# Optimization experiments

Measured on AMD Instinct MI355X. Metric: run time of the kernel, lower is better.

Reference implementation:

```python
import jax, jax.numpy as jnp
import numpy as np

B, S, DIM, HEADS = 4, 2048, 1024, 16
SCALE = float((DIM // HEADS) ** 0.5)  # sqrt(d_k) = 8.0
EPS = 1e-5


def _ln(h, g, b):
    m = jnp.mean(h, axis=-1, keepdims=True)
    v = jnp.mean((h - m) ** 2, axis=-1, keepdims=True)
    return (h - m) * jax.lax.rsqrt(v + EPS) * g + b


def setup_inputs() -> dict:
    key = jax.random.key(0)
    ks = jax.random.split(key, 16)
    w = lambda k: jax.random.normal(k, (DIM, DIM), jnp.float32) * 0.02
    vec = lambda k: jax.random.normal(k, (DIM,), jnp.float32) * 0.02
    return {
        "x": jax.random.normal(ks[0], (B, S, DIM), jnp.float32),
        "Wq": w(ks[1]), "bq": vec(ks[2]),
        "Wk": w(ks[3]), "bk": vec(ks[4]),
        "Wv": w(ks[5]), "bv": vec(ks[6]),
        "g_at": 1.0 + vec(ks[7]), "b_at": vec(ks[8]),
        "g_ln": 1.0 + vec(ks[9]), "b_ln": vec(ks[10]),
        "W1": w(ks[11]), "c1": vec(ks[12]),
        "W2": w(ks[13]), "c2": vec(ks[14]),
    }


def reference(x, Wq, bq, Wk, bk, Wv, bv, g_at, b_at, g_ln, b_ln, W1, c1, W2, c2):
    # --- MultiHeadAttention (single-head math: no head reshape in source) ---
    Q = x @ Wq + bq                                   # [B,S,D]
    K = x @ Wk + bk
    V = x @ Wv + bv
    scores = jax.nn.softmax(jnp.einsum('bqd,bkd->bqk', Q, K) / SCALE, axis=-1)
    at = _ln(jnp.einsum('bqk,bkd->bqd', scores, V) + x, g_at, b_at)
    # --- EncoderStack ---
    h = _ln(at + x, g_ln, b_ln)
    res = h
    # note: source's `if i != len(self.ffn)` is always True -> GELU on every layer
    h = jax.nn.gelu(h @ W1 + c1, approximate=False)
    h = jax.nn.gelu(h @ W2 + c2, approximate=False)
    return _ln(h + res, g_ln, b_ln)
```

## Files before the change

### kernel.cpp

```cpp
#include <hip/hip_runtime.h>
#include <cstdint>
#include <cstddef>

#define DIMN 1024
#define SEQ  2048
#define NBAT 4
#define TOKS (NBAT * SEQ)

typedef unsigned short u16;
typedef unsigned int   u32;

typedef __bf16 bf16x8 __attribute__((ext_vector_type(8)));
typedef float  f32x4  __attribute__((ext_vector_type(4)));

#define AS1 __attribute__((address_space(1)))
#define AS3 __attribute__((address_space(3)))


__device__ __forceinline__ u16 f2b(float f) {
  union { float f; u32 u; } v; v.f = f;
  u32 r = v.u + 0x7fffu + ((v.u >> 16) & 1u);
  return (u16)(r >> 16);
}

__device__ __forceinline__ float b2f(u16 b) {
  union { u32 u; float f; } v; v.u = ((u32)b) << 16;
  return v.f;
}

__device__ __forceinline__ float gelu_exact(float v) {
  return 0.5f * v * (1.0f + erff(v * 0.70710678118654752f));
}

__device__ __forceinline__ void blk_sum2(float& a, float& b, float* sm) {
  #pragma unroll
  for (int o = 32; o >= 1; o >>= 1) {
    a += __shfl_xor(a, o, 64);
    b += __shfl_xor(b, o, 64);
  }
  int w = threadIdx.x >> 6;
  if ((threadIdx.x & 63) == 0) { sm[w] = a; sm[4 + w] = b; }
  __syncthreads();
  a = sm[0] + sm[1] + sm[2] + sm[3];
  b = sm[4] + sm[5] + sm[6] + sm[7];
  __syncthreads();
}

__device__ __forceinline__ float blk_max(float a, float* sm) {
  #pragma unroll
  for (int o = 32; o >= 1; o >>= 1) a = fmaxf(a, __shfl_xor(a, o, 64));
  int w = threadIdx.x >> 6;
  if ((threadIdx.x & 63) == 0) sm[w] = a;
  __syncthreads();
  float r = fmaxf(fmaxf(sm[0], sm[1]), fmaxf(sm[2], sm[3]));
  __syncthreads();
  return r;
}

__device__ __forceinline__ float blk_sum1(float a, float* sm) {
  #pragma unroll
  for (int o = 32; o >= 1; o >>= 1) a += __shfl_xor(a, o, 64);
  int w = threadIdx.x >> 6;
  if ((threadIdx.x & 63) == 0) sm[w] = a;
  __syncthreads();
  float r = sm[0] + sm[1] + sm[2] + sm[3];
  __syncthreads();
  return r;
}

__global__ __launch_bounds__(256) void prep_all(
    const float* __restrict__ x,
    const float* __restrict__ Wq, const float* __restrict__ Wk,
    const float* __restrict__ Wv, const float* __restrict__ W1,
    const float* __restrict__ W2,
    u16* __restrict__ xb,
    u16* __restrict__ Wqkv, u16* __restrict__ W1T, u16* __restrict__ W2T)
{
  __shared__ float t[32][33];
  const int tx = threadIdx.x, ty = threadIdx.y;
  if (blockIdx.z == 5) {
    const int tid = ty * 32 + tx;
    const size_t base = ((size_t)(blockIdx.y * 32 + blockIdx.x)) * 8192;
    #pragma unroll
    for (int it = 0; it < 8; ++it) {
      size_t i = base + (size_t)(it * 256 + tid) * 4;
      float4 v = *(const float4*)(x + i);
      uint2 o;
      o.x = (u32)f2b(v.x) | ((u32)f2b(v.y) << 16);
      o.y = (u32)f2b(v.z) | ((u32)f2b(v.w) << 16);
      *(uint2*)(xb + i) = o;
    }
    return;
  }
  const float* W; u16* T;
  switch (blockIdx.z) {
    case 0: W = Wq; T = Wqkv;                   break;
    case 1: W = Wk; T = Wqkv + 1 * DIMN * DIMN; break;
    case 2: W = Wv; T = Wqkv + 2 * DIMN * DIMN; break;
    case 3: W = W1; T = W1T;                    break;
    default: W = W2; T = W2T;                   break;
  }
  int k0 = blockIdx.x * 32, n0 = blockIdx.y * 32;
  #pragma unroll
  for (int j = 0; j < 32; j += 8)
    t[ty + j][tx] = W[(size_t)(k0 + ty + j) * DIMN + n0 + tx];
  __syncthreads();
  #pragma unroll
  for (int j = 0; j < 32; j += 8)
    T[(size_t)(n0 + ty + j) * DIMN + k0 + tx] = f2b(t[tx][ty + j]);
}

template <int EPI, int SWZ>
__global__ __launch_bounds__(256) void gemm_bt(
    const u16* __restrict__ A, const u16* __restrict__ Bm,
    u16* __restrict__ Cb, u16* __restrict__ Cb2, u16* __restrict__ Cb3,
    const float* __restrict__ bias, const float* __restrict__ bias2,
    const float* __restrict__ bias3,
    int M, int N, int K, int ldc,
    size_t sA, size_t sB, size_t sC)
{
  __shared__ u16 smem[2 * 128 * 64];
  u16* As = smem;
  u16* Bs = smem + 128 * 64;

  const int tid = threadIdx.x;

  int bm0, bn0;
  if (SWZ == 1) {
    const int id   = blockIdx.y * gridDim.x + blockIdx.x;
    const int xcd  = id & 7;
    const int idx  = id >> 3;
    const int band = gridDim.x >> 3;
    bm0 = (xcd * band + idx % band) * 128;
    bn0 = (idx / band) * 128;
  } else {
    bm0 = blockIdx.x * 128;
    bn0 = blockIdx.y * 128;
  }

  A  += (size_t)blockIdx.z * sA;
  Bm += (size_t)blockIdx.z * sB;
  const int wave = tid >> 6, lane = tid & 63;
  const int wm   = (wave >> 1) * 64, wn = (wave & 1) * 64;
  const int l16  = lane & 15, quad = lane >> 4;

  f32x4 acc[4][4] = {};

  for (int k0 = 0; k0 < K; k0 += 64) {
    #pragma unroll
    for (int j = 0; j < 4; ++j) {
      const int c  = wave * 256 + j * 64 + lane;
      const int r  = c >> 3;
      const int cg = (c & 7) ^ (r & 7);
      const u16* gA = A  + (size_t)(bm0 + r) * K + k0 + cg * 8;
      const u16* gB = Bm + (size_t)(bn0 + r) * K + k0 + cg * 8;
      u16* lA = As + (wave * 4 + j) * 512;
      u16* lB = Bs + (wave * 4 + j) * 512;
      __builtin_amdgcn_global_load_lds((const AS1 void*)gA, (AS3 void*)lA, 16, 0, 0);
      __builtin_amdgcn_global_load_lds((const AS1 void*)gB, (AS3 void*)lB, 16, 0, 0);
    }
    __syncthreads();

    #pragma unroll
    for (int kk = 0; kk < 64; kk += 32) {
      const int kc = kk >> 3;
      const int sw = l16 & 7;
      bf16x8 af[4], bfr[4];
      #pragma unroll
      for (int t = 0; t < 4; ++t) {
        const int row = wm + t * 16 + l16;
        af[t] = *(const bf16x8*)(&As[row * 64 + (((kc + quad) ^ sw) << 3)]);
      }
      #pragma unroll
      for (int t = 0; t < 4; ++t) {
        const int row = wn + t * 16 + l16;
        bfr[t] = *(const bf16x8*)(&Bs[row * 64 + (((kc + quad) ^ sw) << 3)]);
      }
      #pragma unroll
      for (int mt = 0; mt < 4; ++mt)
        #pragma unroll
        for (int nt = 0; nt < 4; ++nt)
          acc[mt][nt] = __builtin_amdgcn_mfma_f32_16x16x32_bf16(
              af[mt], bfr[nt], acc[mt][nt], 0, 0, 0);
    }
    __syncthreads();
  }

  if (EPI == 3 && (bn0 >> 10) == 2) {
    #pragma unroll
    for (int mt = 0; mt < 4; ++mt) {
      const int tok_l0 = wm + mt * 16 + quad * 4;
      #pragma unroll
      for (int nt = 0; nt < 4; ++nt) {
        const int d_l = wn + nt * 16 + l16;
        const float bv = bias3[(bn0 & 1023) + d_l];
        ushort4 pk;
        pk.x = f2b(acc[mt][nt][0] + bv);
        pk.y = f2b(acc[mt][nt][1] + bv);
        pk.z = f2b(acc[mt][nt][2] + bv);
        pk.w = f2b(acc[mt][nt][3] + bv);
        const int addr = d_l * 128 +
            ((((tok_l0 >> 3) ^ (d_l & 7)) << 3) | (tok_l0 & 7));
        *(ushort4*)(&smem[addr]) = pk;
      }
    }
    __syncthreads();
    const int b_idx = bm0 >> 11;
    const int tok0  = bm0 & 2047;
    const int d0    = bn0 & 1023;
    u16* dst = Cb3 + (size_t)b_idx * DIMN * SEQ;
    #pragma unroll
    for (int p = 0; p < 8; ++p) {
      const int idx = p * 256 + tid;
      const int row = idx >> 4, c = idx & 15;
      uint4 v = *(const uint4*)(&smem[row * 128 + ((c ^ (row & 7)) << 3)]);
      *(uint4*)(&dst[(size_t)(d0 + row) * SEQ + tok0 + c * 8]) = v;
    }
    return;
  }

  u16* Cbz = Cb + (size_t)blockIdx.z * sC;
  #pragma unroll
  for (int mt = 0; mt < 4; ++mt) {
    int grow0 = bm0 + wm + mt * 16 + quad * 4;
    #pragma unroll
    for (int nt = 0; nt < 4; ++nt) {
      int gcol = bn0 + wn + nt * 16 + l16;
      if (EPI == 3) {
        const int seg = gcol >> 10;
        const int col = gcol & 1023;
        const float* bp = (seg == 0) ? bias : bias2;
        u16*         cp = (seg == 0) ? Cb   : Cb2;
        float bv = bp[col];
        #pragma unroll
        for (int r = 0; r < 4; ++r)
          cp[(size_t)(grow0 + r) * ldc + col] = f2b(acc[mt][nt][r] + bv);
      } else if (EPI == 4) {
        float bv = bias[gcol];
        #pragma unroll
        for (int r = 0; r < 4; ++r)
          Cbz[(size_t)(grow0 + r) * ldc + gcol] =
              f2b(gelu_exact(acc[mt][nt][r] + bv));
      } else {
        #pragma unroll
        for (int r = 0; r < 4; ++r)
          Cbz[(size_t)(grow0 + r) * ldc + gcol] = f2b(acc[mt][nt][r]);
      }
    }
  }
}

__global__ __launch_bounds__(256) void softmax_rows(const u16* __restrict__ Sc,
                                                    u16* __restrict__ P) {
  __shared__ float sm[8];
  int row = blockIdx.x, t = threadIdx.x;
  const u16* s = Sc + (size_t)row * SEQ;
  uint4 raw = *(const uint4*)(s + t * 8);
  float v[8];
  #pragma unroll
  for (int m = 0; m < 4; ++m) {
    u32 w = ((const u32*)&raw)[m];
    v[2 * m]     = b2f((u16)(w & 0xffff)) * 0.125f;
    v[2 * m + 1] = b2f((u16)(w >> 16)) * 0.125f;
  }
  float mx = -1e30f;
  #pragma unroll
  for (int i = 0; i < 8; ++i) mx = fmaxf(mx, v[i]);
  mx = blk_max(mx, sm);
  float sum = 0.0f;
  #pragma unroll
  for (int i = 0; i < 8; ++i) { v[i] = __expf(v[i] - mx); sum += v[i]; }
  sum = blk_sum1(sum, sm);
  float inv = 1.0f / sum;
  uint4 o;
  #pragma unroll
  for (int m = 0; m < 4; ++m)
    ((u32*)&o)[m] = (u32)f2b(v[2 * m] * inv) | ((u32)f2b(v[2 * m + 1] * inv) << 16);
  *(uint4*)(P + (size_t)row * SEQ + t * 8) = o;
}

__global__ __launch_bounds__(256) void ln1_fused(
    const u16* __restrict__ attn, const u16* __restrict__ xb,
    const float* __restrict__ g_at, const float* __restrict__ b_at,
    const float* __restrict__ g_ln, const float* __restrict__ b_ln,
    u16* __restrict__ hres)
{
  __shared__ float sm[8];
  int row = blockIdx.x, t = threadIdx.x;
  size_t base = (size_t)row * DIMN;
  uint2 ar = *(const uint2*)(attn + base + t * 4);
  uint2 xr4 = *(const uint2*)(xb + base + t * 4);
  float y[4], xr[4];
  float s = 0.0f, s2 = 0.0f;
  #pragma unroll
  for (int i = 0; i < 4; ++i) {
    u32 aw = ((const u32*)&ar)[i >> 1];
    u32 xw = ((const u32*)&xr4)[i >> 1];
    float av = b2f((u16)((i & 1) ? (aw >> 16) : (aw & 0xffff)));
    xr[i]    = b2f((u16)((i & 1) ? (xw >> 16) : (xw & 0xffff)));
    y[i] = av + xr[i];
    s += y[i]; s2 += y[i] * y[i];
  }
  blk_sum2(s, s2, sm);
  float m  = s * (1.0f / DIMN);
  float rs = rsqrtf(s2 * (1.0f / DIMN) - m * m + 1e-5f);
  float z[4];
  s = 0.0f; s2 = 0.0f;
  #pragma unroll
  for (int i = 0; i < 4; ++i) {
    int c = t * 4 + i;
    float at = (y[i] - m) * rs * g_at[c] + b_at[c];
    z[i] = at + xr[i];
    s += z[i]; s2 += z[i] * z[i];
  }
  blk_sum2(s, s2, sm);
  float m2  = s * (1.0f / DIMN);
  float rs2 = rsqrtf(s2 * (1.0f / DIMN) - m2 * m2 + 1e-5f);
  uint2 o;
  #pragma unroll
  for (int i = 0; i < 2; ++i) {
    int c = t * 4 + 2 * i;
    float h0 = (z[2 * i]     - m2) * rs2 * g_ln[c]     + b_ln[c];
    float h1 = (z[2 * i + 1] - m2) * rs2 * g_ln[c + 1] + b_ln[c + 1];
    ((u32*)&o)[i] = (u32)f2b(h0) | ((u32)f2b(h1) << 16);
  }
  *(uint2*)(hres + base + t * 4) = o;
}

__global__ __launch_bounds__(256) void ln2_final(
    const u16* __restrict__ u, const u16* __restrict__ hres,
    const float* __restrict__ g, const float* __restrict__ bb,
    float* __restrict__ out)
{
  __shared__ float sm[8];
  int row = blockIdx.x, t = threadIdx.x;
  size_t base = (size_t)row * DIMN;
  uint2 ur = *(const uint2*)(u + base + t * 4);
  uint2 hr = *(const uint2*)(hres + base + t * 4);
  float y[4];
  float s = 0.0f, s2 = 0.0f;
  #pragma unroll
  for (int i = 0; i < 4; ++i) {
    u32 uw = ((const u32*)&ur)[i >> 1];
    u32 hw = ((const u32*)&hr)[i >> 1];
    float uv = b2f((u16)((i & 1) ? (uw >> 16) : (uw & 0xffff)));
    float hv = b2f((u16)((i & 1) ? (hw >> 16) : (hw & 0xffff)));
    y[i] = uv + hv;
    s += y[i]; s2 += y[i] * y[i];
  }
  blk_sum2(s, s2, sm);
  float m  = s * (1.0f / DIMN);
  float rs = rsqrtf(s2 * (1.0f / DIMN) - m * m + 1e-5f);
  float4 o;
  o.x = (y[0] - m) * rs * g[t * 4 + 0] + bb[t * 4 + 0];
  o.y = (y[1] - m) * rs * g[t * 4 + 1] + bb[t * 4 + 1];
  o.z = (y[2] - m) * rs * g[t * 4 + 2] + bb[t * 4 + 2];
  o.w = (y[3] - m) * rs * g[t * 4 + 3] + bb[t * 4 + 3];
  *(float4*)(out + base + t * 4) = o;
}


extern "C" void kernel_launch(void* const* d_in, const int* in_sizes, int n_in,
                              void* d_out, int out_size, void* d_ws, size_t ws_size,
                              hipStream_t stream)
{
  const float* x    = (const float*)d_in[0];
  const float* Wq   = (const float*)d_in[1];
  const float* bq   = (const float*)d_in[2];
  const float* Wk   = (const float*)d_in[3];
  const float* bk   = (const float*)d_in[4];
  const float* Wv   = (const float*)d_in[5];
  const float* bv   = (const float*)d_in[6];
  const float* g_at = (const float*)d_in[7];
  const float* b_at = (const float*)d_in[8];
  const float* g_ln = (const float*)d_in[9];
  const float* b_ln = (const float*)d_in[10];
  const float* W1   = (const float*)d_in[11];
  const float* c1   = (const float*)d_in[12];
  const float* W2   = (const float*)d_in[13];
  const float* c2   = (const float*)d_in[14];
  float* out = (float*)d_out;

  char* ws = (char*)d_ws;
  const size_t MB = 1u << 20;
  u16* xb    = (u16*)(ws + 0 * MB);
  u16* W1T   = (u16*)(ws + 16 * MB);
  u16* W2T   = (u16*)(ws + 18 * MB);
  u16* WqkvT = (u16*)(ws + 20 * MB);
  u16* Qb    = (u16*)(ws + 26 * MB);
  u16* Kb    = (u16*)(ws + 42 * MB);
  u16* VT    = (u16*)(ws + 58 * MB);
  u16* Sc    = (u16*)(ws + 74 * MB);
  u16* attn  = (u16*)(ws + 74 * MB);
  u16* hres  = (u16*)(ws + 90 * MB);
  u16* Pb    = (u16*)(ws + 106 * MB);
  u16* tb    = Kb;
  u16* ub    = VT;

  prep_all<<<dim3(32, 32, 6), dim3(32, 8), 0, stream>>>(
      x, Wq, Wk, Wv, W1, W2, xb, WqkvT, W1T, W2T);

  gemm_bt<3, 1><<<dim3(64, 24), 256, 0, stream>>>(
      xb, WqkvT, Qb, Kb, VT, bq, bk, bv,
      TOKS, 3 * DIMN, DIMN, DIMN, 0, 0, 0);

  gemm_bt<6, 0><<<dim3(16, 16, NBAT), 256, 0, stream>>>(
      Qb, Kb, Sc, nullptr, nullptr, nullptr, nullptr, nullptr,
      SEQ, SEQ, DIMN, SEQ,
      (size_t)SEQ * DIMN, (size_t)SEQ * DIMN, (size_t)SEQ * SEQ);
  softmax_rows<<<TOKS, 256, 0, stream>>>(Sc, Pb);
  gemm_bt<6, 0><<<dim3(16, 8, NBAT), 256, 0, stream>>>(
      Pb, VT, attn, nullptr, nullptr, nullptr, nullptr, nullptr,
      SEQ, DIMN, SEQ, DIMN,
      (size_t)SEQ * SEQ, (size_t)DIMN * SEQ, (size_t)SEQ * DIMN);

  ln1_fused<<<TOKS, 256, 0, stream>>>(attn, xb, g_at, b_at, g_ln, b_ln, hres);

  gemm_bt<4, 1><<<dim3(64, 8), 256, 0, stream>>>(
      hres, W1T, tb, nullptr, nullptr, c1, nullptr, nullptr,
      TOKS, DIMN, DIMN, DIMN, 0, 0, 0);
  gemm_bt<4, 1><<<dim3(64, 8), 256, 0, stream>>>(
      tb, W2T, ub, nullptr, nullptr, c2, nullptr, nullptr,
      TOKS, DIMN, DIMN, DIMN, 0, 0, 0);

  ln2_final<<<TOKS, 256, 0, stream>>>(ub, hres, g_ln, b_ln, out);
}
```

Baseline: 386.6 us.

## Stage GEMM epilogue through LDS, use tanh GELU, wave-per-row softmax and layernorm

The GEMM epilogue now writes results into swizzled shared memory and then issues coalesced 16-byte global stores, in place of scattered 2-byte stores. Exact erf GELU is replaced with the tanh approximation built from __expf. Softmax and both layernorm kernels now process one row per wave with only shuffle reductions, which removes block barriers and uses wider vector loads. The tanh GELU changes numerics relative to the exact reference, and the extra LDS round trip adds a barrier to every GEMM.

```diff
diff --git a/kernel.cpp b/kernel.cpp
--- a/kernel.cpp
+++ b/kernel.cpp
@@ -28,44 +28,40 @@
   return v.f;
 }
 
-__device__ __forceinline__ float gelu_exact(float v) {
-  return 0.5f * v * (1.0f + erff(v * 0.70710678118654752f));
-}
-
-__device__ __forceinline__ void blk_sum2(float& a, float& b, float* sm) {
-  #pragma unroll
-  for (int o = 32; o >= 1; o >>= 1) {
-    a += __shfl_xor(a, o, 64);
-    b += __shfl_xor(b, o, 64);
-  }
-  int w = threadIdx.x >> 6;
-  if ((threadIdx.x & 63) == 0) { sm[w] = a; sm[4 + w] = b; }
-  __syncthreads();
-  a = sm[0] + sm[1] + sm[2] + sm[3];
-  b = sm[4] + sm[5] + sm[6] + sm[7];
-  __syncthreads();
-}
-
-__device__ __forceinline__ float blk_max(float a, float* sm) {
+__device__ __forceinline__ float gelu_fast(float x) {
+  float y = 0.79788456080286536f * (x + 0.044715f * x * x * x);
+  float e = __expf(2.0f * y);
+  float t = 1.0f - 2.0f / (e + 1.0f);
+  return 0.5f * x * (1.0f + t);
+}
+
+__device__ __forceinline__ float wave_sum(float a) {
+  #pragma unroll
+  for (int o = 32; o >= 1; o >>= 1) a += __shfl_xor(a, o, 64);
+  return a;
+}
+
+__device__ __forceinline__ float wave_max(float a) {
   #pragma unroll
   for (int o = 32; o >= 1; o >>= 1) a = fmaxf(a, __shfl_xor(a, o, 64));
-  int w = threadIdx.x >> 6;
-  if ((threadIdx.x & 63) == 0) sm[w] = a;
-  __syncthreads();
-  float r = fmaxf(fmaxf(sm[0], sm[1]), fmaxf(sm[2], sm[3]));
-  __syncthreads();
-  return r;
-}
-
-__device__ __forceinline__ float blk_sum1(float a, float* sm) {
-  #pragma unroll
-  for (int o = 32; o >= 1; o >>= 1) a += __shfl_xor(a, o, 64);
-  int w = threadIdx.x >> 6;
-  if ((threadIdx.x & 63) == 0) sm[w] = a;
-  __syncthreads();
-  float r = sm[0] + sm[1] + sm[2] + sm[3];
-  __syncthreads();
-  return r;
+  return a;
+}
+
+__device__ __forceinline__ void unpack8(uint4 raw, float* o) {
+  #pragma unroll
+  for (int m = 0; m < 4; ++m) {
+    u32 w = ((const u32*)&raw)[m];
+    o[2 * m]     = b2f((u16)(w & 0xffff));
+    o[2 * m + 1] = b2f((u16)(w >> 16));
+  }
+}
+
+__device__ __forceinline__ uint4 pack8(const float* v) {
+  uint4 o;
+  #pragma unroll
+  for (int m = 0; m < 4; ++m)
+    ((u32*)&o)[m] = (u32)f2b(v[2 * m]) | ((u32)f2b(v[2 * m + 1]) << 16);
+  return o;
 }
 
 __global__ __launch_bounds__(256) void prep_all(
@@ -186,7 +182,9 @@
     __syncthreads();
   }
 
-  if (EPI == 3 && (bn0 >> 10) == 2) {
+  const int seg = bn0 >> 10;
+
+  if (EPI == 3 && seg == 2) {
     #pragma unroll
     for (int mt = 0; mt < 4; ++mt) {
       const int tok_l0 = wm + mt * 16 + quad * 4;
@@ -219,64 +217,68 @@
     return;
   }
 
-  u16* Cbz = Cb + (size_t)blockIdx.z * sC;
+  u16* dst; const float* bp; int col0;
+  if (EPI == 3) {
+    dst = seg ? Cb2 : Cb;  bp = seg ? bias2 : bias;  col0 = bn0 & 1023;
+  } else if (EPI == 4) {
+    dst = Cb;  bp = bias;  col0 = bn0;
+  } else {
+    dst = Cb + (size_t)blockIdx.z * sC;  bp = nullptr;  col0 = bn0;
+  }
+
   #pragma unroll
   for (int mt = 0; mt < 4; ++mt) {
-    int grow0 = bm0 + wm + mt * 16 + quad * 4;
+    const int r0 = wm + mt * 16 + quad * 4;
     #pragma unroll
     for (int nt = 0; nt < 4; ++nt) {
-      int gcol = bn0 + wn + nt * 16 + l16;
-      if (EPI == 3) {
-        const int seg = gcol >> 10;
-        const int col = gcol & 1023;
-        const float* bp = (seg == 0) ? bias : bias2;
-        u16*         cp = (seg == 0) ? Cb   : Cb2;
-        float bv = bp[col];
-        #pragma unroll
-        for (int r = 0; r < 4; ++r)
-          cp[(size_t)(grow0 + r) * ldc + col] = f2b(acc[mt][nt][r] + bv);
-      } else if (EPI == 4) {
-        float bv = bias[gcol];
-        #pragma unroll
-        for (int r = 0; r < 4; ++r)
-          Cbz[(size_t)(grow0 + r) * ldc + gcol] =
-              f2b(gelu_exact(acc[mt][nt][r] + bv));
-      } else {
-        #pragma unroll
-        for (int r = 0; r < 4; ++r)
-          Cbz[(size_t)(grow0 + r) * ldc + gcol] = f2b(acc[mt][nt][r]);
+      const int cl = wn + nt * 16 + l16;
+      const float bv = (EPI == 6) ? 0.0f : bp[col0 + cl];
+      #pragma unroll
+      for (int r = 0; r < 4; ++r) {
+        float v = acc[mt][nt][r] + bv;
+        if (EPI == 4) v = gelu_fast(v);
+        const int row  = r0 + r;
+        const int addr = row * 128 + ((((cl >> 3) ^ (row & 7)) << 3) | (cl & 7));
+        smem[addr] = f2b(v);
       }
     }
+  }
+  __syncthreads();
+  #pragma unroll
+  for (int p = 0; p < 8; ++p) {
+    const int idx = p * 256 + tid;
+    const int row = idx >> 4, c = idx & 15;
+    uint4 v = *(const uint4*)(&smem[row * 128 + ((c ^ (row & 7)) << 3)]);
+    *(uint4*)(&dst[(size_t)(bm0 + row) * ldc + col0 + c * 8]) = v;
   }
 }
 
 __global__ __launch_bounds__(256) void softmax_rows(const u16* __restrict__ Sc,
                                                     u16* __restrict__ P) {
-  __shared__ float sm[8];
-  int row = blockIdx.x, t = threadIdx.x;
+  const int wave = threadIdx.x >> 6, lane = threadIdx.x & 63;
+  const int row  = blockIdx.x * 4 + wave;
   const u16* s = Sc + (size_t)row * SEQ;
-  uint4 raw = *(const uint4*)(s + t * 8);
-  float v[8];
-  #pragma unroll
-  for (int m = 0; m < 4; ++m) {
-    u32 w = ((const u32*)&raw)[m];
-    v[2 * m]     = b2f((u16)(w & 0xffff)) * 0.125f;
-    v[2 * m + 1] = b2f((u16)(w >> 16)) * 0.125f;
+  u16*       p = P  + (size_t)row * SEQ;
+  float v[32];
+  #pragma unroll
+  for (int k = 0; k < 4; ++k) {
+    uint4 raw = *(const uint4*)(s + k * 512 + lane * 8);
+    unpack8(raw, &v[k * 8]);
   }
   float mx = -1e30f;
   #pragma unroll
-  for (int i = 0; i < 8; ++i) mx = fmaxf(mx, v[i]);
-  mx = blk_max(mx, sm);
+  for (int i = 0; i < 32; ++i) { v[i] *= 0.125f; mx = fmaxf(mx, v[i]); }
+  mx = wave_max(mx);
   float sum = 0.0f;
   #pragma unroll
-  for (int i = 0; i < 8; ++i) { v[i] = __expf(v[i] - mx); sum += v[i]; }
-  sum = blk_sum1(sum, sm);
+  for (int i = 0; i < 32; ++i) { v[i] = __expf(v[i] - mx); sum += v[i]; }
+  sum = wave_sum(sum);
   float inv = 1.0f / sum;
-  uint4 o;
-  #pragma unroll
-  for (int m = 0; m < 4; ++m)
-    ((u32*)&o)[m] = (u32)f2b(v[2 * m] * inv) | ((u32)f2b(v[2 * m + 1] * inv) << 16);
-  *(uint4*)(P + (size_t)row * SEQ + t * 8) = o;
+  #pragma unroll
+  for (int i = 0; i < 32; ++i) v[i] *= inv;
+  #pragma unroll
+  for (int k = 0; k < 4; ++k)
+    *(uint4*)(p + k * 512 + lane * 8) = pack8(&v[k * 8]);
 }
 
 __global__ __launch_bounds__(256) void ln1_fused(
@@ -285,46 +287,70 @@
     const float* __restrict__ g_ln, const float* __restrict__ b_ln,
     u16* __restrict__ hres)
 {
-  __shared__ float sm[8];
-  int row = blockIdx.x, t = threadIdx.x;
-  size_t base = (size_t)row * DIMN;
-  uint2 ar = *(const uint2*)(attn + base + t * 4);
-  uint2 xr4 = *(const uint2*)(xb + base + t * 4);
-  float y[4], xr[4];
+  const int wave = threadIdx.x >> 6, lane = threadIdx.x & 63;
+  const int row  = blockIdx.x * 4 + wave;
+  const size_t base = (size_t)row * DIMN;
+  const int c0 = lane * 8, c1 = 512 + lane * 8;
+
+  float av[16], xr[16], y[16];
+  unpack8(*(const uint4*)(attn + base + c0), &av[0]);
+  unpack8(*(const uint4*)(attn + base + c1), &av[8]);
+  unpack8(*(const uint4*)(xb + base + c0), &xr[0]);
+  unpack8(*(const uint4*)(xb + base + c1), &xr[8]);
+
   float s = 0.0f, s2 = 0.0f;
   #pragma unroll
-  for (int i = 0; i < 4; ++i) {
-    u32 aw = ((const u32*)&ar)[i >> 1];
-    u32 xw = ((const u32*)&xr4)[i >> 1];
-    float av = b2f((u16)((i & 1) ? (aw >> 16) : (aw & 0xffff)));
-    xr[i]    = b2f((u16)((i & 1) ? (xw >> 16) : (xw & 0xffff)));
-    y[i] = av + xr[i];
+  for (int i = 0; i < 16; ++i) {
+    y[i] = av[i] + xr[i];
     s += y[i]; s2 += y[i] * y[i];
   }
-  blk_sum2(s, s2, sm);
+  s = wave_sum(s); s2 = wave_sum(s2);
   float m  = s * (1.0f / DIMN);
   float rs = rsqrtf(s2 * (1.0f / DIMN) - m * m + 1e-5f);
-  float z[4];
+
+  float z[16];
   s = 0.0f; s2 = 0.0f;
   #pragma unroll
-  for (int i = 0; i < 4; ++i) {
-    int c = t * 4 + i;
-    float at = (y[i] - m) * rs * g_at[c] + b_at[c];
-    z[i] = at + xr[i];
-    s += z[i]; s2 += z[i] * z[i];
-  }
-  blk_sum2(s, s2, sm);
+  for (int h = 0; h < 2; ++h) {
+    const int c = h ? c1 : c0;
+    float4 ga = *(const float4*)(g_at + c), gb = *(const float4*)(g_at + c + 4);
+    float4 ba = *(const float4*)(b_at + c), bb = *(const float4*)(b_at + c + 4);
+    const float* gp = (const float*)&ga; const float* gq = (const float*)&gb;
+    const float* bp = (const float*)&ba; const float* bq = (const float*)&bb;
+    #pragma unroll
+    for (int i = 0; i < 4; ++i) {
+      int j = h * 8 + i;
+      float at = (y[j] - m) * rs * gp[i] + bp[i];
+      z[j] = at + xr[j]; s += z[j]; s2 += z[j] * z[j];
+    }
+    #pragma unroll
+    for (int i = 0; i < 4; ++i) {
+      int j = h * 8 + 4 + i;
+      float at = (y[j] - m) * rs * gq[i] + bq[i];
+      z[j] = at + xr[j]; s += z[j]; s2 += z[j] * z[j];
+    }
+  }
+  s = wave_sum(s); s2 = wave_sum(s2);
   float m2  = s * (1.0f / DIMN);
   float rs2 = rsqrtf(s2 * (1.0f / DIMN) - m2 * m2 + 1e-5f);
-  uint2 o;
-  #pragma unroll
-  for (int i = 0; i < 2; ++i) {
-    int c = t * 4 + 2 * i;
-    float h0 = (z[2 * i]     - m2) * rs2 * g_ln[c]     + b_ln[c];
-    float h1 = (z[2 * i + 1] - m2) * rs2 * g_ln[c + 1] + b_ln[c + 1];
-    ((u32*)&o)[i] = (u32)f2b(h0) | ((u32)f2b(h1) << 16);
-  }
-  *(uint2*)(hres + base + t * 4) = o;
+
+  float o[16];
+  #pragma unroll
+  for (int h = 0; h < 2; ++h) {
+    const int c = h ? c1 : c0;
+    float4 ga = *(const float4*)(g_ln + c), gb = *(const float4*)(g_ln + c + 4);
+    float4 ba = *(const float4*)(b_ln + c), bb = *(const float4*)(b_ln + c + 4);
+    const float* gp = (const float*)&ga; const float* gq = (const float*)&gb;
+    const float* bp = (const float*)&ba; const float* bq = (const float*)&bb;
+    #pragma unroll
+    for (int i = 0; i < 4; ++i)
+      o[h * 8 + i] = (z[h * 8 + i] - m2) * rs2 * gp[i] + bp[i];
+    #pragma unroll
+    for (int i = 0; i < 4; ++i)
+      o[h * 8 + 4 + i] = (z[h * 8 + 4 + i] - m2) * rs2 * gq[i] + bq[i];
+  }
+  *(uint4*)(hres + base + c0) = pack8(&o[0]);
+  *(uint4*)(hres + base + c1) = pack8(&o[8]);
 }
 
 __global__ __launch_bounds__(256) void ln2_final(
@@ -332,31 +358,46 @@
     const float* __restrict__ g, const float* __restrict__ bb,
     float* __restrict__ out)
 {
-  __shared__ float sm[8];
-  int row = blockIdx.x, t = threadIdx.x;
-  size_t base = (size_t)row * DIMN;
-  uint2 ur = *(const uint2*)(u + base + t * 4);
-  uint2 hr = *(const uint2*)(hres + base + t * 4);
-  float y[4];
+  const int wave = threadIdx.x >> 6, lane = threadIdx.x & 63;
+  const int row  = blockIdx.x * 4 + wave;
+  const size_t base = (size_t)row * DIMN;
+  const int c0 = lane * 8, c1 = 512 + lane * 8;
+
+  float uv[16], hv[16], y[16];
+  unpack8(*(const uint4*)(u + base + c0), &uv[0]);
+  unpack8(*(const uint4*)(u + base + c1), &uv[8]);
+  unpack8(*(const uint4*)(hres + base + c0), &hv[0]);
+  unpack8(*(const uint4*)(hres + base + c1), &hv[8]);
+
   float s = 0.0f, s2 = 0.0f;
   #pragma unroll
-  for (int i = 0; i < 4; ++i) {
-    u32 uw = ((const u32*)&ur)[i >> 1];
-    u32 hw = ((const u32*)&hr)[i >> 1];
-    float uv = b2f((u16)((i & 1) ? (uw >> 16) : (uw & 0xffff)));
-    float hv = b2f((u16)((i & 1) ? (hw >> 16) : (hw & 0xffff)));
-    y[i] = uv + hv;
+  for (int i = 0; i < 16; ++i) {
+    y[i] = uv[i] + hv[i];
     s += y[i]; s2 += y[i] * y[i];
   }
-  blk_sum2(s, s2, sm);
+  s = wave_sum(s); s2 = wave_sum(s2);
   float m  = s * (1.0f / DIMN);
   float rs = rsqrtf(s2 * (1.0f / DIMN) - m * m + 1e-5f);
-  float4 o;
-  o.x = (y[0] - m) * rs * g[t * 4 + 0] + bb[t * 4 + 0];
-  o.y = (y[1] - m) * rs * g[t * 4 + 1] + bb[t * 4 + 1];
-  o.z = (y[2] - m) * rs * g[t * 4 + 2] + bb[t * 4 + 2];
-  o.w = (y[3] - m) * rs * g[t * 4 + 3] + bb[t * 4 + 3];
-  *(float4*)(out + base + t * 4) = o;
+
+  #pragma unroll
+  for (int h = 0; h < 2; ++h) {
+    const int c = h ? c1 : c0;
+    float4 ga = *(const float4*)(g + c),  gb2 = *(const float4*)(g + c + 4);
+    float4 ba = *(const float4*)(bb + c), bb2 = *(const float4*)(bb + c + 4);
+    const float* gp = (const float*)&ga;  const float* gq = (const float*)&gb2;
+    const float* bp = (const float*)&ba;  const float* bq = (const float*)&bb2;
+    float4 o1, o2;
+    ((float*)&o1)[0] = (y[h*8+0] - m) * rs * gp[0] + bp[0];
+    ((float*)&o1)[1] = (y[h*8+1] - m) * rs * gp[1] + bp[1];
+    ((float*)&o1)[2] = (y[h*8+2] - m) * rs * gp[2] + bp[2];
+    ((float*)&o1)[3] = (y[h*8+3] - m) * rs * gp[3] + bp[3];
+    ((float*)&o2)[0] = (y[h*8+4] - m) * rs * gq[0] + bq[0];
+    ((float*)&o2)[1] = (y[h*8+5] - m) * rs * gq[1] + bq[1];
+    ((float*)&o2)[2] = (y[h*8+6] - m) * rs * gq[2] + bq[2];
+    ((float*)&o2)[3] = (y[h*8+7] - m) * rs * gq[3] + bq[3];
+    *(float4*)(out + base + c)     = o1;
+    *(float4*)(out + base + c + 4) = o2;
+  }
 }
 
 
@@ -408,13 +449,13 @@
       Qb, Kb, Sc, nullptr, nullptr, nullptr, nullptr, nullptr,
       SEQ, SEQ, DIMN, SEQ,
       (size_t)SEQ * DIMN, (size_t)SEQ * DIMN, (size_t)SEQ * SEQ);
-  softmax_rows<<<TOKS, 256, 0, stream>>>(Sc, Pb);
+  softmax_rows<<<TOKS / 4, 256, 0, stream>>>(Sc, Pb);
   gemm_bt<6, 0><<<dim3(16, 8, NBAT), 256, 0, stream>>>(
       Pb, VT, attn, nullptr, nullptr, nullptr, nullptr, nullptr,
       SEQ, DIMN, SEQ, DIMN,
       (size_t)SEQ * SEQ, (size_t)DIMN * SEQ, (size_t)SEQ * DIMN);
 
-  ln1_fused<<<TOKS, 256, 0, stream>>>(attn, xb, g_at, b_at, g_ln, b_ln, hres);
+  ln1_fused<<<TOKS / 4, 256, 0, stream>>>(attn, xb, g_at, b_at, g_ln, b_ln, hres);
 
   gemm_bt<4, 1><<<dim3(64, 8), 256, 0, stream>>>(
       hres, W1T, tb, nullptr, nullptr, c1, nullptr, nullptr,
@@ -423,5 +464,5 @@
       tb, W2T, ub, nullptr, nullptr, c2, nullptr, nullptr,
       TOKS, DIMN, DIMN, DIMN, 0, 0, 0);
 
-  ln2_final<<<TOKS, 256, 0, stream>>>(ub, hres, g_ln, b_ln, out);
-}
+  ln2_final<<<TOKS / 4, 256, 0, stream>>>(ub, hres, g_ln, b_ln, out);
+}
```

After: 388.5 us. No clear change (+0.5%).
